# Kernel optimization log

Hardware: AMD Instinct MI355X
Metric: run time of the kernel (lower is better)

Reference implementation:

```python
import jax, jax.numpy as jnp
import numpy as np

N, TO, TI, H = 8, 2048, 2048, 128
MASK_FILL = -99999.0  # module uses -99999.0, not -inf


def setup_inputs() -> dict:
    key = jax.random.key(0)
    kq, kv, km = jax.random.split(key, 3)
    queries = jax.random.normal(kq, (N, TO, H), dtype=jnp.float32)
    values = jax.random.normal(kv, (N, TI, H), dtype=jnp.float32)
    # mask is applied to scores.view(-1, Ti) -> shape (N*To, Ti), True = masked
    mask = jax.random.randint(km, (N * TO, TI), 0, 2).astype(bool)
    return {"queries": queries, "values": values, "mask": mask}


def reference(queries, values, mask):
    n, to, h = queries.shape
    ti = values.shape[1]
    # N x To x Ti scores (no 1/sqrt(H) scaling in the original)
    scores = jnp.einsum("nth,nsh->nts", queries, values)
    scores = jnp.where(mask.reshape(n, to, ti), MASK_FILL, scores)
    attention_distribution = jax.nn.softmax(scores, axis=-1)
    attention_output = jnp.einsum("nts,nsh->nth", attention_distribution, values)
    return attention_output, attention_distribution
```

## Files before the change

### kernel.cpp

```cpp
#include <hip/hip_runtime.h>

#define NB  8
#define TOQ 2048
#define TIV 2048
#define HD  128

typedef float f32x4 __attribute__((ext_vector_type(4)));
typedef short s16x8 __attribute__((ext_vector_type(8)));
typedef unsigned short ushort8v __attribute__((ext_vector_type(8)));

__device__ __forceinline__ unsigned short f2bf(float f) {
    unsigned u = __float_as_uint(f);
    return (unsigned short)((u + 0x7FFFu + ((u >> 16) & 1u)) >> 16);
}
__device__ __forceinline__ float bf2f(unsigned short h) {
    return __uint_as_float(((unsigned)h) << 16);
}

__device__ __forceinline__ void split8(const float4 a, const float4 b,
                                       ushort8v& h, ushort8v& l) {
    const float x[8] = {a.x, a.y, a.z, a.w, b.x, b.y, b.z, b.w};
    #pragma unroll
    for (int j = 0; j < 8; ++j) {
        const unsigned short hi = f2bf(x[j]);
        h[j] = hi;
        l[j] = f2bf(x[j] - bf2f(hi));
    }
}

__global__ __launch_bounds__(256) void k0_vt(
    const float* __restrict__ V, unsigned short* __restrict__ VT)
{
    __shared__ unsigned short tile[64][68];
    const int n  = blockIdx.z;
    const int s0 = blockIdx.x * 64;
    const int h0 = blockIdx.y * 64;
    const int t  = threadIdx.x;

    #pragma unroll
    for (int it = 0; it < 4; ++it) {
        const int f = t + it * 256;
        const int r = f >> 4;
        const int c = f & 15;
        const float4 v = *(const float4*)&V[((size_t)(n * TIV + s0 + r)) * HD + h0 + 4 * c];
        tile[4 * c + 0][r] = f2bf(v.x);
        tile[4 * c + 1][r] = f2bf(v.y);
        tile[4 * c + 2][r] = f2bf(v.z);
        tile[4 * c + 3][r] = f2bf(v.w);
    }
    __syncthreads();

    #pragma unroll
    for (int it = 0; it < 2; ++it) {
        const int f  = t + it * 256;
        const int hh = f >> 3;
        const int sc = f & 7;
        ushort8v o;
        #pragma unroll
        for (int j = 0; j < 8; ++j) o[j] = tile[hh][8 * sc + j];
        *(ushort8v*)&VT[((size_t)(n * HD + h0 + hh)) * TIV + s0 + 8 * sc] = o;
    }
}

__global__ __launch_bounds__(256) void k1_mfma(
    const float* __restrict__ Q, const float* __restrict__ V,
    const int* __restrict__ M, float* __restrict__ E,
    float* __restrict__ part)
{
    __shared__ unsigned short qhi[128 * 32], qlo[128 * 32];
    __shared__ unsigned short vhi[128 * 32], vlo[128 * 32];

    const int n    = blockIdx.z;
    const int tt   = blockIdx.y * 128;
    const int ts   = blockIdx.x * 128;
    const int t    = threadIdx.x;
    const int lane = t & 63;
    const int wave = t >> 6;
    const int wr   = wave >> 1;
    const int wc   = wave & 1;
    const int lr   = lane & 15;
    const int kg   = lane >> 4;

    const float* Qb = Q + ((size_t)n * TOQ + tt) * HD;
    const float* Vb = V + ((size_t)n * TIV + ts) * HD;

    f32x4 acc[4][4];
    #pragma unroll
    for (int i = 0; i < 4; ++i)
        #pragma unroll
        for (int j = 0; j < 4; ++j) acc[i][j] = (f32x4)0.f;

    for (int h0 = 0; h0 < HD; h0 += 32) {
        #pragma unroll
        for (int it = 0; it < 2; ++it) {
            const int i   = t + it * 256;
            const int row = i >> 2;
            const int kb  = i & 3;
            const float* qs = Qb + (size_t)row * HD + h0 + kb * 8;
            const float* vs = Vb + (size_t)row * HD + h0 + kb * 8;
            const float4 q0 = *(const float4*)qs, q1 = *(const float4*)(qs + 4);
            const float4 v0 = *(const float4*)vs, v1 = *(const float4*)(vs + 4);
            ushort8v qh, ql, vh, vl;
            split8(q0, q1, qh, ql);
            split8(v0, v1, vh, vl);
            *(ushort8v*)(qhi + i * 8) = qh;
            *(ushort8v*)(qlo + i * 8) = ql;
            *(ushort8v*)(vhi + i * 8) = vh;
            *(ushort8v*)(vlo + i * 8) = vl;
        }
        __syncthreads();

        s16x8 aH[4], aL[4];
        #pragma unroll
        for (int fm = 0; fm < 4; ++fm) {
            const int off = (wr * 64 + fm * 16 + lr) * 32 + kg * 8;
            aH[fm] = *(const s16x8*)(vhi + off);
            aL[fm] = *(const s16x8*)(vlo + off);
        }
        #pragma unroll
        for (int fn = 0; fn < 4; ++fn) {
            const int off = (wc * 64 + fn * 16 + lr) * 32 + kg * 8;
            const s16x8 bH = *(const s16x8*)(qhi + off);
            const s16x8 bL = *(const s16x8*)(qlo + off);
            #pragma unroll
            for (int fm = 0; fm < 4; ++fm) {
                acc[fm][fn] = __builtin_amdgcn_mfma_f32_16x16x32_bf16(aH[fm], bH, acc[fm][fn], 0, 0, 0);
                acc[fm][fn] = __builtin_amdgcn_mfma_f32_16x16x32_bf16(aH[fm], bL, acc[fm][fn], 0, 0, 0);
                acc[fm][fn] = __builtin_amdgcn_mfma_f32_16x16x32_bf16(aL[fm], bH, acc[fm][fn], 0, 0, 0);
            }
        }
        __syncthreads();
    }

    #pragma unroll
    for (int fn = 0; fn < 4; ++fn) {
        const int to_g = tt + wc * 64 + fn * 16 + lr;
        const size_t rowbase = ((size_t)n * TOQ + to_g) * TIV;
        float rs = 0.f;
        #pragma unroll
        for (int fm = 0; fm < 4; ++fm) {
            const int ti_g = ts + wr * 64 + fm * 16 + kg * 4;
            const int4 mv = *(const int4*)&M[rowbase + ti_g];
            float4 e;
            e.x = mv.x ? 0.f : __expf(acc[fm][fn][0]);
            e.y = mv.y ? 0.f : __expf(acc[fm][fn][1]);
            e.z = mv.z ? 0.f : __expf(acc[fm][fn][2]);
            e.w = mv.w ? 0.f : __expf(acc[fm][fn][3]);
            *(float4*)&E[rowbase + ti_g] = e;
            rs += (e.x + e.y) + (e.z + e.w);
        }
        rs += __shfl_xor(rs, 16, 64);
        rs += __shfl_xor(rs, 32, 64);
        if (kg == 0)
            part[((size_t)n * TOQ + to_g) * 32 + blockIdx.x * 2 + wr] = rs;
    }
}

__global__ __launch_bounds__(256) void k2_rowsum(
    const float* __restrict__ part, float* __restrict__ rec)
{
    const int row = blockIdx.x * 256 + threadIdx.x;
    const float4* p4 = (const float4*)(part + (size_t)row * 32);
    float s = 0.f;
    #pragma unroll
    for (int i = 0; i < 8; ++i) {
        const float4 v = p4[i];
        s += (v.x + v.y) + (v.z + v.w);
    }
    rec[row] = 1.f / s;
}

__global__ __launch_bounds__(512) void k3_pv(
    float* __restrict__ EP, const unsigned short* __restrict__ VT,
    const float* __restrict__ rec, float* __restrict__ O)
{
    __shared__ float red[2][3][16][132];

    const int n    = blockIdx.y;
    const int r0   = blockIdx.x * 32;
    const int t    = threadIdx.x;
    const int wave = t >> 6;
    const int lane = t & 63;
    const int p    = wave >> 2;
    const int q    = wave & 3;
    const int lr   = lane & 15;
    const int kg   = lane >> 4;

    const int rowg = r0 + p * 16 + lr;
    const float rc = rec[n * TOQ + rowg];
    float* Erow = EP + ((size_t)n * TOQ + rowg) * TIV;
    const unsigned short* VTb = VT + (size_t)n * HD * TIV;

    f32x4 acc[8];
    #pragma unroll
    for (int fn = 0; fn < 8; ++fn) acc[fn] = (f32x4)0.f;

    const int kbase = q * 512 + kg * 8;

    #pragma unroll 2
    for (int k0 = 0; k0 < 512; k0 += 32) {
        const int k = kbase + k0;
        const float4 e0 = *(const float4*)&Erow[k];
        const float4 e1 = *(const float4*)&Erow[k + 4];
        float4 p0, p1;
        p0.x = e0.x * rc; p0.y = e0.y * rc; p0.z = e0.z * rc; p0.w = e0.w * rc;
        p1.x = e1.x * rc; p1.y = e1.y * rc; p1.z = e1.z * rc; p1.w = e1.w * rc;
        *(float4*)&Erow[k]     = p0;
        *(float4*)&Erow[k + 4] = p1;

        s16x8 a;
        a[0] = (short)f2bf(p0.x); a[1] = (short)f2bf(p0.y);
        a[2] = (short)f2bf(p0.z); a[3] = (short)f2bf(p0.w);
        a[4] = (short)f2bf(p1.x); a[5] = (short)f2bf(p1.y);
        a[6] = (short)f2bf(p1.z); a[7] = (short)f2bf(p1.w);

        #pragma unroll
        for (int fn = 0; fn < 8; ++fn) {
            const s16x8 b = *(const s16x8*)&VTb[(size_t)(fn * 16 + lr) * TIV + k];
            acc[fn] = __builtin_amdgcn_mfma_f32_16x16x32_bf16(a, b, acc[fn], 0, 0, 0);
        }
    }

    if (q != 0) {
        #pragma unroll
        for (int fn = 0; fn < 8; ++fn)
            #pragma unroll
            for (int ri = 0; ri < 4; ++ri)
                red[p][q - 1][kg * 4 + ri][fn * 16 + lr] = acc[fn][ri];
    }
    __syncthreads();
    if (q == 0) {
        #pragma unroll
        for (int fn = 0; fn < 8; ++fn) {
            #pragma unroll
            for (int ri = 0; ri < 4; ++ri) {
                const int orow = r0 + p * 16 + kg * 4 + ri;
                float o = acc[fn][ri];
                o += red[p][0][kg * 4 + ri][fn * 16 + lr];
                o += red[p][1][kg * 4 + ri][fn * 16 + lr];
                o += red[p][2][kg * 4 + ri][fn * 16 + lr];
                O[((size_t)n * TOQ + orow) * HD + fn * 16 + lr] = o;
            }
        }
    }
}

extern "C" void kernel_launch(void* const* d_in, const int* in_sizes, int n_in,
                              void* d_out, int out_size, void* d_ws, size_t ws_size,
                              hipStream_t stream)
{
    const float* Q = (const float*)d_in[0];
    const float* V = (const float*)d_in[1];
    const int*   M = (const int*)d_in[2];

    float* O = (float*)d_out;
    float* E = O + (size_t)NB * TOQ * HD;

    float*          recb = (float*)d_ws;
    float*          part = (float*)((char*)d_ws + (1 << 16));
    unsigned short* VT   = (unsigned short*)((char*)d_ws + (1 << 16) + (NB * TOQ * 32 * 4));

    k0_vt    <<<dim3(TIV / 64, HD / 64, NB), 256, 0, stream>>>(V, VT);
    k1_mfma  <<<dim3(TIV / 128, TOQ / 128, NB), 256, 0, stream>>>(Q, V, M, E, part);
    k2_rowsum<<<dim3(NB * TOQ / 256), 256, 0, stream>>>(part, recb);
    k3_pv    <<<dim3(TOQ / 32, NB), 512, 0, stream>>>(E, VT, recb, O);
}
```

Baseline: 184.2 us.

## Pre-split Q/V into bf16 hi/lo and stage QK tiles via direct global-to-LDS loads

Adds a pre-pass that splits Q and V once into bf16 high and low halves stored in workspace. The score kernel then loads these pre-split tiles straight into LDS with global_load_lds instead of converting fp32 inside every block. This removes the redundant split work that each tile repeated and frees VGPRs used for staging. The cost is an extra kernel launch plus more workspace traffic, and the new path runs only when the workspace is large enough; otherwise it falls back to the old kernel.

```diff
diff --git a/kernel.cpp b/kernel.cpp
--- a/kernel.cpp
+++ b/kernel.cpp
@@ -26,6 +26,29 @@
         h[j] = hi;
         l[j] = f2bf(x[j] - bf2f(hi));
     }
+}
+
+__device__ __forceinline__ void gload16(const void* g, void* l) {
+    __builtin_amdgcn_global_load_lds(
+        (const __attribute__((address_space(1))) void*)g,
+        (__attribute__((address_space(3))) void*)l, 16, 0, 0);
+}
+
+__global__ __launch_bounds__(256) void k0_split(
+    const float* __restrict__ Q, const float* __restrict__ V,
+    unsigned short* __restrict__ Qh, unsigned short* __restrict__ Ql,
+    unsigned short* __restrict__ Vh, unsigned short* __restrict__ Vl)
+{
+    const size_t i = ((size_t)blockIdx.x * 256 + threadIdx.x) * 8;
+    const float* src = blockIdx.y ? V : Q;
+    unsigned short* dh = blockIdx.y ? Vh : Qh;
+    unsigned short* dl = blockIdx.y ? Vl : Ql;
+    const float4 a = *(const float4*)&src[i];
+    const float4 b = *(const float4*)&src[i + 4];
+    ushort8v h, l;
+    split8(a, b, h, l);
+    *(ushort8v*)&dh[i] = h;
+    *(ushort8v*)&dl[i] = l;
 }
 
 __global__ __launch_bounds__(256) void k0_vt(
@@ -62,7 +85,95 @@
     }
 }
 
-__global__ __launch_bounds__(256) void k1_mfma(
+__global__ __launch_bounds__(256) void k1_lds(
+    const unsigned short* __restrict__ QhG, const unsigned short* __restrict__ QlG,
+    const unsigned short* __restrict__ VhG, const unsigned short* __restrict__ VlG,
+    const int* __restrict__ M, float* __restrict__ E,
+    float* __restrict__ part)
+{
+    __shared__ unsigned short qh_l[128 * 32], ql_l[128 * 32];
+    __shared__ unsigned short vh_l[128 * 32], vl_l[128 * 32];
+
+    const int n    = blockIdx.z;
+    const int tt   = blockIdx.y * 128;
+    const int ts   = blockIdx.x * 128;
+    const int t    = threadIdx.x;
+    const int lane = t & 63;
+    const int wave = t >> 6;
+    const int wr   = wave >> 1;
+    const int wc   = wave & 1;
+    const int lr   = lane & 15;
+    const int kg   = lane >> 4;
+
+    f32x4 acc[4][4];
+    #pragma unroll
+    for (int i = 0; i < 4; ++i)
+        #pragma unroll
+        for (int j = 0; j < 4; ++j) acc[i][j] = (f32x4)0.f;
+
+    for (int h0 = 0; h0 < HD; h0 += 32) {
+        #pragma unroll
+        for (int j = 0; j < 2; ++j) {
+            const int c    = wave * 128 + j * 64 + lane;
+            const int row  = c >> 2;
+            const int kb   = (c & 3) * 8;
+            const int lb   = (wave * 128 + j * 64) * 8;
+            const size_t qo = ((size_t)(n * TOQ + tt + row)) * HD + h0 + kb;
+            const size_t vo = ((size_t)(n * TIV + ts + row)) * HD + h0 + kb;
+            gload16(QhG + qo, qh_l + lb);
+            gload16(QlG + qo, ql_l + lb);
+            gload16(VhG + vo, vh_l + lb);
+            gload16(VlG + vo, vl_l + lb);
+        }
+        __syncthreads();
+
+        s16x8 aH[4], aL[4];
+        #pragma unroll
+        for (int fm = 0; fm < 4; ++fm) {
+            const int off = (wr * 64 + fm * 16 + lr) * 32 + kg * 8;
+            aH[fm] = *(const s16x8*)(vh_l + off);
+            aL[fm] = *(const s16x8*)(vl_l + off);
+        }
+        #pragma unroll
+        for (int fn = 0; fn < 4; ++fn) {
+            const int off = (wc * 64 + fn * 16 + lr) * 32 + kg * 8;
+            const s16x8 bH = *(const s16x8*)(qh_l + off);
+            const s16x8 bL = *(const s16x8*)(ql_l + off);
+            #pragma unroll
+            for (int fm = 0; fm < 4; ++fm) {
+                acc[fm][fn] = __builtin_amdgcn_mfma_f32_16x16x32_bf16(aH[fm], bH, acc[fm][fn], 0, 0, 0);
+                acc[fm][fn] = __builtin_amdgcn_mfma_f32_16x16x32_bf16(aH[fm], bL, acc[fm][fn], 0, 0, 0);
+                acc[fm][fn] = __builtin_amdgcn_mfma_f32_16x16x32_bf16(aL[fm], bH, acc[fm][fn], 0, 0, 0);
+            }
+        }
+        __syncthreads();
+    }
+
+    #pragma unroll
+    for (int fn = 0; fn < 4; ++fn) {
+        const int to_g = tt + wc * 64 + fn * 16 + lr;
+        const size_t rowbase = ((size_t)n * TOQ + to_g) * TIV;
+        float rs = 0.f;
+        #pragma unroll
+        for (int fm = 0; fm < 4; ++fm) {
+            const int ti_g = ts + wr * 64 + fm * 16 + kg * 4;
+            const int4 mv = *(const int4*)&M[rowbase + ti_g];
+            float4 e;
+            e.x = mv.x ? 0.f : __expf(acc[fm][fn][0]);
+            e.y = mv.y ? 0.f : __expf(acc[fm][fn][1]);
+            e.z = mv.z ? 0.f : __expf(acc[fm][fn][2]);
+            e.w = mv.w ? 0.f : __expf(acc[fm][fn][3]);
+            *(float4*)&E[rowbase + ti_g] = e;
+            rs += (e.x + e.y) + (e.z + e.w);
+        }
+        rs += __shfl_xor(rs, 16, 64);
+        rs += __shfl_xor(rs, 32, 64);
+        if (kg == 0)
+            part[((size_t)n * TOQ + to_g) * 32 + blockIdx.x * 2 + wr] = rs;
+    }
+}
+
+__global__ __launch_bounds__(256) void k1_reg(
     const float* __restrict__ Q, const float* __restrict__ V,
     const int* __restrict__ M, float* __restrict__ E,
     float* __restrict__ part)
@@ -256,12 +367,29 @@
     float* O = (float*)d_out;
     float* E = O + (size_t)NB * TOQ * HD;
 
-    float*          recb = (float*)d_ws;
-    float*          part = (float*)((char*)d_ws + (1 << 16));
-    unsigned short* VT   = (unsigned short*)((char*)d_ws + (1 << 16) + (NB * TOQ * 32 * 4));
-
-    k0_vt    <<<dim3(TIV / 64, HD / 64, NB), 256, 0, stream>>>(V, VT);
-    k1_mfma  <<<dim3(TIV / 128, TOQ / 128, NB), 256, 0, stream>>>(Q, V, M, E, part);
+    char* ws = (char*)d_ws;
+    float*          recb = (float*)ws;
+    float*          part = (float*)(ws + (1 << 16));
+    unsigned short* VT   = (unsigned short*)(ws + (1 << 16) + (NB * TOQ * 32 * 4));
+
+    const size_t elems   = (size_t)NB * TOQ * HD;
+    const size_t sbytes  = elems * 2;
+    const size_t base    = (1 << 16) + (size_t)(NB * TOQ * 32 * 4) + sbytes;
+    const size_t ws_need = base + 4 * sbytes;
+
+    k0_vt<<<dim3(TIV / 64, HD / 64, NB), 256, 0, stream>>>(V, VT);
+
+    if (ws_size >= ws_need) {
+        unsigned short* Qh = (unsigned short*)(ws + base);
+        unsigned short* Ql = (unsigned short*)(ws + base + sbytes);
+        unsigned short* Vh = (unsigned short*)(ws + base + 2 * sbytes);
+        unsigned short* Vl = (unsigned short*)(ws + base + 3 * sbytes);
+        k0_split<<<dim3((unsigned)(elems / 8 / 256), 2), 256, 0, stream>>>(Q, V, Qh, Ql, Vh, Vl);
+        k1_lds  <<<dim3(TIV / 128, TOQ / 128, NB), 256, 0, stream>>>(Qh, Ql, Vh, Vl, M, E, part);
+    } else {
+        k1_reg  <<<dim3(TIV / 128, TOQ / 128, NB), 256, 0, stream>>>(Q, V, M, E, part);
+    }
+
     k2_rowsum<<<dim3(NB * TOQ / 256), 256, 0, stream>>>(part, recb);
     k3_pv    <<<dim3(TOQ / 32, NB), 512, 0, stream>>>(E, VT, recb, O);
 }
```

After: 185.8 us. Within noise of the previous version (+0.9%).
